# Optimization experiments

Hardware: AMD Instinct MI355X
Metric: run time of the kernel (lower is better)

## Reference

```python
import jax, jax.numpy as jnp
import numpy as np

H = 256            # hidden_size
S = 4              # num_of_steps
B = 512            # reactions
N_MOLS = B * S     # 2048 molecules
ATOMS_PER_MOL = 32
N_ATOMS = N_MOLS * ATOMS_PER_MOL   # 65536
BONDS_PER_MOL = 64
N_BONDS = N_MOLS * BONDS_PER_MOL   # 131072 directed bonds (+1 pad row)
MAX_NB = 6
ATOM_FDIM = 133
BOND_FDIM = 147
DEPTH = 3
N_ITERS = 3  # Set2Set iterations


def setup_inputs() -> dict:
    key = jax.random.key(0)
    ks = jax.random.split(key, 20)
    def p(k, shape):
        return jax.random.normal(k, shape, jnp.float32) * 0.02
    inp = {}
    inp['f_atoms'] = jax.random.normal(ks[0], (N_ATOMS, ATOM_FDIM), jnp.float32)
    f_bonds = jax.random.normal(ks[1], (N_BONDS + 1, BOND_FDIM), jnp.float32)
    inp['f_bonds'] = f_bonds.at[0].set(0.0)  # chemprop zero pad row
    inp['a2b'] = jax.random.randint(ks[2], (N_ATOMS, MAX_NB), 0, N_BONDS + 1)
    inp['b2a'] = jax.random.randint(ks[3], (N_BONDS + 1,), 0, N_ATOMS)
    inp['b2revb'] = jax.random.randint(ks[4], (N_BONDS + 1,), 0, N_BONDS + 1)
    # MPN weights (bias=False for W_i/W_h as in args.bias default)
    inp['W_i'] = p(ks[5], (BOND_FDIM, H))
    inp['W_h'] = p(ks[6], (H, H))
    inp['W_o'] = p(ks[7], (ATOM_FDIM + H, H)); inp['b_o'] = jnp.zeros((H,), jnp.float32)
    # NNAttention over steps
    inp['W_nn0'] = p(ks[8], (2 * H, H));  inp['b_nn0'] = jnp.zeros((H,), jnp.float32)
    inp['W_nn0s'] = p(ks[9], (H, H));     inp['b_nn0s'] = jnp.zeros((H,), jnp.float32)
    inp['W_nn1'] = p(ks[10], (S * H, H)); inp['b_nn1'] = jnp.zeros((H,), jnp.float32)
    # node Set2Set (LSTM: input 2H -> hidden H) + condenser
    inp['lstm_n_Wih'] = p(ks[11], (4 * H, 2 * H))
    inp['lstm_n_Whh'] = p(ks[12], (4 * H, H))
    inp['lstm_n_b'] = jnp.zeros((4 * H,), jnp.float32)
    inp['node_cond_W'] = p(ks[13], (2 * H, H)); inp['node_cond_b'] = jnp.zeros((H,), jnp.float32)
    # graph (step) Set2Set + condenser
    inp['lstm_g_Wih'] = p(ks[14], (4 * H, 2 * H))
    inp['lstm_g_Whh'] = p(ks[15], (4 * H, H))
    inp['lstm_g_b'] = jnp.zeros((4 * H,), jnp.float32)
    inp['graph_cond_W'] = p(ks[16], (2 * H, H)); inp['graph_cond_b'] = jnp.zeros((H,), jnp.float32)
    return inp


def set2set(feat, Wih, Whh, b):
    # feat: [M, N, D]; LSTM n_layers=1, PyTorch gate order i,f,g,o
    M, N, D = feat.shape
    h = jnp.zeros((M, D), feat.dtype)
    c = jnp.zeros((M, D), feat.dtype)
    q_star = jnp.zeros((M, 2 * D), feat.dtype)
    for _ in range(N_ITERS):
        gates = q_star @ Wih.T + h @ Whh.T + b
        i, f, g, o = jnp.split(gates, 4, axis=-1)
        c = jax.nn.sigmoid(f) * c + jax.nn.sigmoid(i) * jnp.tanh(g)
        h = jax.nn.sigmoid(o) * jnp.tanh(c)
        q = h
        alpha = jax.nn.softmax(jnp.einsum('md,mnd->mn', q, feat), axis=1)
        readout = jnp.einsum('mn,mnd->md', alpha, feat)
        q_star = jnp.concatenate([q, readout], axis=-1)
    return q_star


def nn_attention(h, W0, b0, W0s, b0s, W1, b1):
    # vectorized form of the Attention module's s1/s2 double loop
    Bm, Sm, D = h.shape
    h1 = jnp.broadcast_to(h[:, :, None, :], (Bm, Sm, Sm, D))
    h2 = jnp.broadcast_to(h[:, None, :, :], (Bm, Sm, Sm, D))
    pair = jnp.concatenate([h1, h2], -1) @ W0 + b0          # [B,S,S,D] NN0(cat(h_s1,h_s2))
    self_o = h @ W0s + b0s                                   # [B,S,D]   NN0_self(h_s1)
    diag = jnp.eye(Sm, dtype=bool)[None, :, :, None]
    out = jnp.where(diag, self_o[:, :, None, :], pair)       # diagonal uses NN0_self
    return out.reshape(Bm, Sm, Sm * D) @ W1 + b1             # NN1 over s2-concat


def reference(f_atoms, f_bonds, a2b, b2a, b2revb, W_i, W_h, W_o, b_o,
              W_nn0, b_nn0, W_nn0s, b_nn0s, W_nn1, b_nn1,
              lstm_n_Wih, lstm_n_Whh, lstm_n_b, node_cond_W, node_cond_b,
              lstm_g_Wih, lstm_g_Whh, lstm_g_b, graph_cond_W, graph_cond_b):
    # --- bond message passing (chemprop, atom_messages=False) ---
    inp = f_bonds @ W_i                       # [NB+1, H], row 0 = 0 (no bias)
    message = jax.nn.relu(inp)
    message = message.at[0].set(0.0)          # keep pad row zero
    for _ in range(DEPTH - 1):
        a_message = message[a2b].sum(axis=1)          # gather+sum: [NA, H]
        msg = a_message[b2a] - message[b2revb]        # [NB+1, H]
        message = jax.nn.relu(inp + msg @ W_h)
        message = message.at[0].set(0.0)
    nei = message[a2b].sum(axis=1)                    # [NA, H]
    atom_h = jax.nn.relu(jnp.concatenate([f_atoms, nei], -1) @ W_o + b_o)
    # --- node readout: Set2Set per molecule + condenser ---
    feat = atom_h.reshape(N_MOLS, ATOMS_PER_MOL, H)
    mol = set2set(feat, lstm_n_Wih, lstm_n_Whh, lstm_n_b) @ node_cond_W + node_cond_b
    # --- step attention (NNAttention over num_of_steps) ---
    steps = mol.reshape(B, S, H)
    steps = nn_attention(steps, W_nn0, b_nn0, W_nn0s, b_nn0s, W_nn1, b_nn1)
    # --- step readout: Set2Set over steps + condenser ---
    out = set2set(steps, lstm_g_Wih, lstm_g_Whh, lstm_g_b) @ graph_cond_W + graph_cond_b
    return out  # [B, H]
```

## Files before the change

kernel.cpp:

```cpp
#include <hip/hip_runtime.h>
#include <math.h>

#define H 256
#define S_STEPS 4
#define B_RXN 512
#define N_MOLS 2048
#define ATOMS_PER_MOL 32
#define N_ATOMS 65536
#define N_BONDS 131072
#define NBP1 131073
#define MAX_NB 6
#define ATOM_FDIM 133
#define BOND_FDIM 147
#define DEPTH 3
#define N_ITERS 3

typedef unsigned short bf16u;
typedef __attribute__((ext_vector_type(8))) short short8v;
typedef __attribute__((ext_vector_type(4))) float f32x4;

__device__ __forceinline__ float b2f(bf16u u) {
    union { unsigned int i; float f; } c; c.i = ((unsigned int)u) << 16; return c.f;
}
__device__ __forceinline__ bf16u f2b(float f) {
    union { float f; unsigned int i; } c; c.f = f;
    unsigned int i = c.i;
    return (bf16u)((i + 0x7FFFu + ((i >> 16) & 1u)) >> 16);
}
__device__ __forceinline__ unsigned int relu2bf(unsigned int w) {
    unsigned int lo = w & 0xFFFFu, hi = w >> 16;
    if (lo & 0x8000u) lo = 0u;
    if (hi & 0x8000u) hi = 0u;
    return lo | (hi << 16);
}

template<int MODE, bool RELUA>
__global__ __launch_bounds__(512) void dense_gemm_k(
    const bf16u* __restrict__ A1,
    const bf16u* __restrict__ A2,
    const bf16u* __restrict__ WT,
    const float* __restrict__ bias,
    bf16u* __restrict__ outb,
    int M)
{
    constexpr int KP = (MODE == 0) ? 160 : ((MODE == 1) ? 256 : 416);
    __shared__ bf16u As[128][40];
    __shared__ bf16u Bs[256][40];

    const int tid = threadIdx.x;
    const int lane = tid & 63, w = tid >> 6;
    const int wr = w >> 2, wc = w & 3;
    const int m0 = blockIdx.x * 128;
    const int ar = tid >> 2, q8 = (tid & 3) * 8;
    const int br = tid >> 1, bh = (tid & 1) * 16;
    const int arow = m0 + ar;
    const bool rok = arow < M;
    const int lr = lane & 15, lk = (lane >> 4) * 8;
    const uint4 z4 = {0u, 0u, 0u, 0u};

    f32x4 acc[4][4];
    const f32x4 zf = {0.f, 0.f, 0.f, 0.f};
    #pragma unroll
    for (int i = 0; i < 4; ++i)
        #pragma unroll
        for (int j = 0; j < 4; ++j) acc[i][j] = zf;

    for (int k0 = 0; k0 < KP; k0 += 32) {
        const int kc = k0 + q8;
        uint4 va;
        if (MODE == 2) {
            va = (kc < 160) ? *(const uint4*)(A1 + (size_t)arow * 160 + kc)
                            : *(const uint4*)(A2 + (size_t)arow * 256 + (kc - 160));
        } else {
            constexpr int LDA = (MODE == 0) ? 160 : 256;
            va = rok ? *(const uint4*)(A1 + (size_t)arow * LDA + kc) : z4;
        }
        if (RELUA) {
            va.x = relu2bf(va.x); va.y = relu2bf(va.y);
            va.z = relu2bf(va.z); va.w = relu2bf(va.w);
        }
        *(uint4*)&As[ar][q8] = va;
        {
            const bf16u* bp = WT + (size_t)br * KP + k0 + bh;
            uint4 b0 = *(const uint4*)(bp);
            uint4 b1 = *(const uint4*)(bp + 8);
            *(uint4*)&Bs[br][bh] = b0;
            *(uint4*)&Bs[br][bh + 8] = b1;
        }
        __syncthreads();

        short8v a[4], b[4];
        #pragma unroll
        for (int mf = 0; mf < 4; ++mf)
            a[mf] = *(const short8v*)&As[wr * 64 + mf * 16 + lr][lk];
        #pragma unroll
        for (int nf = 0; nf < 4; ++nf)
            b[nf] = *(const short8v*)&Bs[wc * 64 + nf * 16 + lr][lk];
        #pragma unroll
        for (int mf = 0; mf < 4; ++mf)
            #pragma unroll
            for (int nf = 0; nf < 4; ++nf)
                acc[mf][nf] = __builtin_amdgcn_mfma_f32_16x16x32_bf16(
                    a[mf], b[nf], acc[mf][nf], 0, 0, 0);
        __syncthreads();
    }

    const int rbase = (lane >> 4) * 4;
    #pragma unroll
    for (int mf = 0; mf < 4; ++mf) {
        #pragma unroll
        for (int nf = 0; nf < 4; ++nf) {
            const int col = wc * 64 + nf * 16 + lr;
            #pragma unroll
            for (int r = 0; r < 4; ++r) {
                const int row = m0 + wr * 64 + mf * 16 + rbase + r;
                if (row >= M) continue;
                float v = acc[mf][nf][r];
                const size_t off = (size_t)row * H + col;
                if (MODE == 2) {
                    v += bias[col];
                    outb[off] = f2b(fmaxf(v, 0.f));
                } else {
                    outb[off] = f2b(v);
                }
            }
        }
    }
}

__global__ __launch_bounds__(256) void combine_k(
    const bf16u* __restrict__ inp, const bf16u* __restrict__ AP,
    const bf16u* __restrict__ MW,
    const int* __restrict__ b2a, const int* __restrict__ b2revb,
    bf16u* __restrict__ msg)
{
    int idx = blockIdx.x * 256 + threadIdx.x;
    if (idx >= NBP1 * 32) return;
    int b = idx >> 5, c = (idx & 31) * 8;
    bf16u* op = msg + (size_t)b * H + c;
    if (b == 0) {
        *(uint4*)op = make_uint4(0u, 0u, 0u, 0u);
        return;
    }
    int a = b2a[b], rb = b2revb[b];
    uint4 ui = *(const uint4*)(inp + (size_t)b * H + c);
    uint4 up = *(const uint4*)(AP + (size_t)a * H + c);
    uint4 um = *(const uint4*)(MW + (size_t)rb * H + c);
    uint4 o;
    unsigned int* pi = &ui.x; unsigned int* pp = &up.x;
    unsigned int* pm = &um.x; unsigned int* po = &o.x;
    #pragma unroll
    for (int t = 0; t < 4; ++t) {
        float lo = b2f((bf16u)(pi[t] & 0xFFFFu)) + b2f((bf16u)(pp[t] & 0xFFFFu))
                 - b2f((bf16u)(pm[t] & 0xFFFFu));
        float hi = b2f((bf16u)(pi[t] >> 16)) + b2f((bf16u)(pp[t] >> 16))
                 - b2f((bf16u)(pm[t] >> 16));
        lo = fmaxf(lo, 0.f); hi = fmaxf(hi, 0.f);
        po[t] = (unsigned int)f2b(lo) | ((unsigned int)f2b(hi) << 16);
    }
    *(uint4*)op = o;
}

template<bool BIAS>
__global__ __launch_bounds__(256) void lin64_k(
    const float* __restrict__ A1, int lda1, int KA1,
    const float* __restrict__ A2, int lda2,
    const bf16u* __restrict__ WT, int ldw,
    const float* __restrict__ bias,
    float* __restrict__ C, int ldc, int K)
{
    __shared__ bf16u As[64][40];
    __shared__ bf16u Bs[64][40];
    const int tid = threadIdx.x;
    const int lane = tid & 63, w = tid >> 6;
    const int m0 = blockIdx.x * 64;
    const int col0 = blockIdx.y * 64;
    const int ar = tid >> 2, kq8 = (tid & 3) * 8;
    const int lr = lane & 15, lk = (lane >> 4) * 8;

    f32x4 acc[4];
    const f32x4 zf = {0.f, 0.f, 0.f, 0.f};
    #pragma unroll
    for (int j = 0; j < 4; ++j) acc[j] = zf;

    for (int k0 = 0; k0 < K; k0 += 32) {
        const float* src = (k0 < KA1)
            ? (A1 + (size_t)(m0 + ar) * lda1 + k0 + kq8)
            : (A2 + (size_t)(m0 + ar) * lda2 + (k0 - KA1) + kq8);
        float4 f0 = *(const float4*)src;
        float4 f1 = *(const float4*)(src + 4);
        ushort4 s0, s1;
        s0.x = f2b(f0.x); s0.y = f2b(f0.y); s0.z = f2b(f0.z); s0.w = f2b(f0.w);
        s1.x = f2b(f1.x); s1.y = f2b(f1.y); s1.z = f2b(f1.z); s1.w = f2b(f1.w);
        *(ushort4*)&As[ar][kq8] = s0;
        *(ushort4*)&As[ar][kq8 + 4] = s1;
        *(uint4*)&Bs[ar][kq8] = *(const uint4*)(WT + (size_t)(col0 + ar) * ldw + k0 + kq8);
        __syncthreads();

        short8v a = *(const short8v*)&As[w * 16 + lr][lk];
        short8v b[4];
        #pragma unroll
        for (int nf = 0; nf < 4; ++nf)
            b[nf] = *(const short8v*)&Bs[nf * 16 + lr][lk];
        #pragma unroll
        for (int nf = 0; nf < 4; ++nf)
            acc[nf] = __builtin_amdgcn_mfma_f32_16x16x32_bf16(a, b[nf], acc[nf], 0, 0, 0);
        __syncthreads();
    }

    const int rbase = (lane >> 4) * 4;
    #pragma unroll
    for (int nf = 0; nf < 4; ++nf) {
        const int col = col0 + nf * 16 + lr;
        #pragma unroll
        for (int r = 0; r < 4; ++r) {
            const int row = m0 + w * 16 + rbase + r;
            float v = acc[nf][r];
            if (BIAS) v += bias[col];
            C[(size_t)row * ldc + col] = v;
        }
    }
}

__global__ __launch_bounds__(256) void prep_wt_k(const float* __restrict__ W,
                                                 bf16u* __restrict__ WT, int K, int KP)
{
    int idx = blockIdx.x * 256 + threadIdx.x;
    if (idx >= 256 * KP) return;
    int n = idx / KP, k = idx - n * KP;
    WT[idx] = (k < K) ? f2b(W[(size_t)k * H + n]) : (bf16u)0;
}

__global__ __launch_bounds__(256) void prep_wto_k(const float* __restrict__ Wo,
                                                  bf16u* __restrict__ WT)
{
    int idx = blockIdx.x * 256 + threadIdx.x;
    if (idx >= 256 * 416) return;
    int n = idx / 416, k = idx - n * 416;
    float v = 0.f;
    if (k < ATOM_FDIM) v = Wo[(size_t)k * H + n];
    else if (k >= 160) v = Wo[(size_t)(ATOM_FDIM + k - 160) * H + n];
    WT[idx] = f2b(v);
}

__global__ __launch_bounds__(256) void prep_wt_t_k(const float* __restrict__ W,
                                                   bf16u* __restrict__ WT, int K)
{
    int idx = blockIdx.x * 256 + threadIdx.x;
    if (idx >= 256 * K) return;
    int n = idx / K, k = idx - n * K;
    WT[idx] = f2b(W[(size_t)k * 256 + n]);
}

__global__ __launch_bounds__(256) void prep_wt_gates_k(const float* __restrict__ Wih,
                                                       const float* __restrict__ Whh,
                                                       bf16u* __restrict__ WT)
{
    int idx = blockIdx.x * 256 + threadIdx.x;
    if (idx >= 1024 * 768) return;
    int n = idx / 768, k = idx - n * 768;
    WT[idx] = f2b(k < 512 ? Wih[(size_t)n * 512 + k] : Whh[(size_t)n * 256 + (k - 512)]);
}

__global__ __launch_bounds__(256) void prep_wt_pqs_k(const float* __restrict__ Wnn0,
                                                     const float* __restrict__ Wnn0s,
                                                     bf16u* __restrict__ WT,
                                                     float* __restrict__ bias_pqs,
                                                     const float* __restrict__ b_nn0s)
{
    int idx = blockIdx.x * 256 + threadIdx.x;
    if (idx < 768) bias_pqs[idx] = (idx < 512) ? 0.f : b_nn0s[idx - 512];
    if (idx >= 768 * 256) return;
    int n = idx / 256, k = idx - n * 256;
    float v;
    if (n < 256)      v = Wnn0[(size_t)k * 256 + n];
    else if (n < 512) v = Wnn0[(size_t)(256 + k) * 256 + (n - 256)];
    else              v = Wnn0s[(size_t)k * 256 + (n - 512)];
    WT[idx] = f2b(v);
}

__global__ __launch_bounds__(256) void prep_feat16_k(const float* __restrict__ F,
                                                     bf16u* __restrict__ O,
                                                     int rows, int K)
{
    int idx = blockIdx.x * 256 + threadIdx.x;
    if (idx >= rows * 160) return;
    int r = idx / 160, c = idx - r * 160;
    O[idx] = (c < K) ? f2b(F[(size_t)r * K + c]) : (bf16u)0;
}

__global__ __launch_bounds__(256) void gather6_bf16_k(const bf16u* __restrict__ msg,
                                                      const int* __restrict__ a2b,
                                                      bf16u* __restrict__ outb)
{
    int idx = blockIdx.x * 256 + threadIdx.x;
    if (idx >= N_ATOMS * (H / 8)) return;
    int na = idx >> 5, c = idx & 31;
    const int* nb = a2b + (size_t)na * MAX_NB;
    float s[8] = {0.f, 0.f, 0.f, 0.f, 0.f, 0.f, 0.f, 0.f};
    #pragma unroll
    for (int j = 0; j < MAX_NB; ++j) {
        uint4 u = *(const uint4*)(msg + (size_t)nb[j] * H + c * 8);
        s[0] += b2f((bf16u)(u.x & 0xFFFFu)); s[1] += b2f((bf16u)(u.x >> 16));
        s[2] += b2f((bf16u)(u.y & 0xFFFFu)); s[3] += b2f((bf16u)(u.y >> 16));
        s[4] += b2f((bf16u)(u.z & 0xFFFFu)); s[5] += b2f((bf16u)(u.z >> 16));
        s[6] += b2f((bf16u)(u.w & 0xFFFFu)); s[7] += b2f((bf16u)(u.w >> 16));
    }
    uint4 o;
    o.x = (unsigned int)f2b(s[0]) | ((unsigned int)f2b(s[1]) << 16);
    o.y = (unsigned int)f2b(s[2]) | ((unsigned int)f2b(s[3]) << 16);
    o.z = (unsigned int)f2b(s[4]) | ((unsigned int)f2b(s[5]) << 16);
    o.w = (unsigned int)f2b(s[6]) | ((unsigned int)f2b(s[7]) << 16);
    *(uint4*)(outb + (size_t)na * H + c * 8) = o;
}

__global__ __launch_bounds__(256) void zero_f32_k(float* __restrict__ p, int n)
{
    int idx = blockIdx.x * 256 + threadIdx.x;
    if (idx < n) p[idx] = 0.f;
}

__device__ __forceinline__ float sigm(float x) { return 1.f / (1.f + expf(-x)); }

__global__ __launch_bounds__(256) void lstm_pw_k(const float* __restrict__ gates,
                                                 float* __restrict__ h,
                                                 float* __restrict__ c, int M)
{
    int idx = blockIdx.x * 256 + threadIdx.x;
    if (idx >= M * H) return;
    int m = idx >> 8, d = idx & 255;
    const float* g = gates + (size_t)m * (4 * H);
    float ig = sigm(g[d]);
    float fg = sigm(g[H + d]);
    float gg = tanhf(g[2 * H + d]);
    float og = sigm(g[3 * H + d]);
    float cn = fg * c[idx] + ig * gg;
    c[idx] = cn;
    h[idx] = og * tanhf(cn);
}

template<bool BF16F>
__global__ __launch_bounds__(256) void s2s_attn_k(const void* __restrict__ featv,
                                                  const float* __restrict__ h,
                                                  float* __restrict__ q_star, int Nn)
{
    int m = blockIdx.x;
    int t = threadIdx.x;
    int lane = t & 63, wave = t >> 6;
    __shared__ float sc[32];
    const bf16u* fb = (const bf16u*)featv;
    const float* ff = (const float*)featv;
    const size_t fbase = (size_t)m * Nn * H;
    const float* hm = h + (size_t)m * H;
    for (int n = wave; n < Nn; n += 4) {
        float p = 0.f;
        if (BF16F) {
            ushort4 u = *(const ushort4*)(fb + fbase + (size_t)n * H + lane * 4);
            const float4 h4 = *(const float4*)(hm + lane * 4);
            p = b2f(u.x) * h4.x + b2f(u.y) * h4.y + b2f(u.z) * h4.z + b2f(u.w) * h4.w;
        } else {
            const float* fr = ff + fbase + (size_t)n * H;
            #pragma unroll
            for (int u = 0; u < 4; ++u) p += fr[lane * 4 + u] * hm[lane * 4 + u];
        }
        #pragma unroll
        for (int o = 32; o >= 1; o >>= 1) p += __shfl_xor(p, o);
        if (lane == 0) sc[n] = p;
    }
    __syncthreads();
    float mx = -1e30f;
    for (int n = 0; n < Nn; ++n) mx = fmaxf(mx, sc[n]);
    float ssum = 0.f, r = 0.f;
    for (int n = 0; n < Nn; ++n) {
        float a = expf(sc[n] - mx);
        ssum += a;
        float fv = BF16F ? b2f(fb[fbase + (size_t)n * H + t]) : ff[fbase + (size_t)n * H + t];
        r += a * fv;
    }
    r /= ssum;
    q_star[(size_t)m * (2 * H) + t] = hm[t];
    q_star[(size_t)m * (2 * H) + H + t] = r;
}

__global__ __launch_bounds__(256) void build_x_k(const float* __restrict__ PQS,
                                                 const float* __restrict__ b0,
                                                 float* __restrict__ X)
{
    int idx = blockIdx.x * 256 + threadIdx.x;
    if (idx >= B_RXN * S_STEPS * S_STEPS * H) return;
    int d  = idx & 255;
    int s2 = (idx >> 8) & 3;
    int s1 = (idx >> 10) & 3;
    int b  = idx >> 12;
    float v;
    if (s1 == s2) v = PQS[((size_t)(b * S_STEPS + s1)) * 768 + 512 + d];
    else v = PQS[((size_t)(b * S_STEPS + s1)) * 768 + d]
           + PQS[((size_t)(b * S_STEPS + s2)) * 768 + 256 + d] + b0[d];
    X[idx] = v;
}

extern "C" void kernel_launch(void* const* d_in, const int* in_sizes, int n_in,
                              void* d_out, int out_size, void* d_ws, size_t ws_size,
                              hipStream_t stream)
{
    const float* f_atoms   = (const float*)d_in[0];
    const float* f_bonds   = (const float*)d_in[1];
    const int*   a2b       = (const int*)d_in[2];
    const int*   b2a       = (const int*)d_in[3];
    const int*   b2revb    = (const int*)d_in[4];
    const float* W_i       = (const float*)d_in[5];
    const float* W_h       = (const float*)d_in[6];
    const float* W_o       = (const float*)d_in[7];
    const float* b_o       = (const float*)d_in[8];
    const float* W_nn0     = (const float*)d_in[9];
    const float* b_nn0     = (const float*)d_in[10];
    const float* W_nn0s    = (const float*)d_in[11];
    const float* b_nn0s    = (const float*)d_in[12];
    const float* W_nn1     = (const float*)d_in[13];
    const float* b_nn1     = (const float*)d_in[14];
    const float* lstm_n_Wih = (const float*)d_in[15];
    const float* lstm_n_Whh = (const float*)d_in[16];
    const float* lstm_n_b   = (const float*)d_in[17];
    const float* node_cond_W = (const float*)d_in[18];
    const float* node_cond_b = (const float*)d_in[19];
    const float* lstm_g_Wih = (const float*)d_in[20];
    const float* lstm_g_Whh = (const float*)d_in[21];
    const float* lstm_g_b   = (const float*)d_in[22];
    const float* graph_cond_W = (const float*)d_in[23];
    const float* graph_cond_b = (const float*)d_in[24];
    float* out = (float*)d_out;

    const size_t SZB = (size_t)NBP1 * H * sizeof(bf16u);
    char* base = (char*)d_ws;
    bf16u* INP  = (bf16u*)(base);
    bf16u* MSG  = (bf16u*)(base + SZB);
    bf16u* MW   = (bf16u*)(base + 2 * SZB);
    bf16u* AMSG = (bf16u*)(base + 3 * SZB);
    bf16u* WT_I = (bf16u*)(base + 3 * SZB + 33554432);
    bf16u* WT_H = (bf16u*)(base + 3 * SZB + 33636352);
    bf16u* WT_O = (bf16u*)(base + 3 * SZB + 33767424);
    bf16u* FB16 = MW;
    bf16u* FA16 = MW;
    bf16u* ATOMH16 = (bf16u*)(base);
    float* SMALL = (float*)(base + SZB);
    float* GATES  = SMALL;
    float* HN     = SMALL + 2097152;
    float* CN     = SMALL + 2621440;
    float* QSTARN = SMALL + 3145728;
    float* MOL    = SMALL + 4194304;
    float* PQS    = SMALL + 4718592;
    float* XBUF   = SMALL + 6291456;
    float* STEPS  = SMALL + 8388608;
    float* HG     = SMALL + 8912896;
    float* CG     = SMALL + 9043968;
    float* QSTARG = SMALL + 9175040;
    float* GATESG = SMALL + 9437184;
    char* sm2 = base + 2 * SZB + 25165824;
    bf16u* WTG_N   = (bf16u*)(sm2);
    bf16u* WTG_G   = (bf16u*)(sm2 + 1572864);
    bf16u* WT_NC   = (bf16u*)(sm2 + 3145728);
    bf16u* WT_PQS  = (bf16u*)(sm2 + 3407872);
    bf16u* WT_N1   = (bf16u*)(sm2 + 3801088);
    bf16u* WT_GC   = (bf16u*)(sm2 + 4325376);
    float* BIAS_PQS = (float*)(sm2 + 4587520);

    dim3 blk(256), blk5(512);
    const int MB_BOND = (NBP1 + 127) / 128;
    const int MB_ATOM = N_ATOMS / 128;
    const int G_GATH = (N_ATOMS * (H / 8) + 255) / 256;
    const int G_COMB = (NBP1 * 32 + 255) / 256;

    prep_wt_k<<<(256 * 160 + 255) / 256, blk, 0, stream>>>(W_i, WT_I, BOND_FDIM, 160);
    prep_wt_k<<<(256 * 256 + 255) / 256, blk, 0, stream>>>(W_h, WT_H, H, 256);
    prep_wto_k<<<(256 * 416 + 255) / 256, blk, 0, stream>>>(W_o, WT_O);
    prep_feat16_k<<<(int)(((size_t)NBP1 * 160 + 255) / 256), blk, 0, stream>>>(
        f_bonds, FB16, NBP1, BOND_FDIM);

    dense_gemm_k<0, false><<<MB_BOND, blk5, 0, stream>>>(
        FB16, nullptr, WT_I, nullptr, INP, NBP1);

    dense_gemm_k<1, true><<<MB_BOND, blk5, 0, stream>>>(
        INP, nullptr, WT_H, nullptr, MW, NBP1);
    gather6_bf16_k<<<G_GATH, blk, 0, stream>>>(MW, a2b, AMSG);
    combine_k<<<G_COMB, blk, 0, stream>>>(INP, AMSG, MW, b2a, b2revb, MSG);
    dense_gemm_k<1, false><<<MB_BOND, blk5, 0, stream>>>(
        MSG, nullptr, WT_H, nullptr, MW, NBP1);
    gather6_bf16_k<<<G_GATH, blk, 0, stream>>>(MW, a2b, AMSG);
    combine_k<<<G_COMB, blk, 0, stream>>>(INP, AMSG, MW, b2a, b2revb, MSG);

    gather6_bf16_k<<<G_GATH, blk, 0, stream>>>(MSG, a2b, AMSG);

    prep_feat16_k<<<(N_ATOMS * 160 + 255) / 256, blk, 0, stream>>>(
        f_atoms, FA16, N_ATOMS, ATOM_FDIM);
    prep_wt_gates_k<<<(1024 * 768 + 255) / 256, blk, 0, stream>>>(lstm_n_Wih, lstm_n_Whh, WTG_N);
    prep_wt_gates_k<<<(1024 * 768 + 255) / 256, blk, 0, stream>>>(lstm_g_Wih, lstm_g_Whh, WTG_G);
    prep_wt_t_k<<<(256 * 512 + 255) / 256, blk, 0, stream>>>(node_cond_W, WT_NC, 512);
    prep_wt_pqs_k<<<(768 * 256 + 255) / 256, blk, 0, stream>>>(W_nn0, W_nn0s, WT_PQS, BIAS_PQS, b_nn0s);
    prep_wt_t_k<<<(256 * 1024 + 255) / 256, blk, 0, stream>>>(W_nn1, WT_N1, 1024);
    prep_wt_t_k<<<(256 * 512 + 255) / 256, blk, 0, stream>>>(graph_cond_W, WT_GC, 512);

    dense_gemm_k<2, false><<<MB_ATOM, blk5, 0, stream>>>(
        FA16, AMSG, WT_O, b_o, ATOMH16, N_ATOMS);

    zero_f32_k<<<(2097152 + 255) / 256, blk, 0, stream>>>(HN, 2097152);
    for (int it = 0; it < N_ITERS; ++it) {
        lin64_k<true><<<dim3(N_MOLS / 64, 16), blk, 0, stream>>>(
            QSTARN, 2 * H, 2 * H, HN, H, WTG_N, 3 * H, lstm_n_b, GATES, 4 * H, 3 * H);
        lstm_pw_k<<<(N_MOLS * H) / 256, blk, 0, stream>>>(GATES, HN, CN, N_MOLS);
        s2s_attn_k<true><<<N_MOLS, blk, 0, stream>>>(ATOMH16, HN, QSTARN, ATOMS_PER_MOL);
    }
    lin64_k<true><<<dim3(N_MOLS / 64, 4), blk, 0, stream>>>(
        QSTARN, 2 * H, 2 * H, QSTARN, 2 * H, WT_NC, 2 * H, node_cond_b, MOL, H, 2 * H);

    lin64_k<true><<<dim3(N_MOLS / 64, 12), blk, 0, stream>>>(
        MOL, H, H, MOL, H, WT_PQS, H, BIAS_PQS, PQS, 3 * H, H);
    build_x_k<<<(B_RXN * 16 * H) / 256, blk, 0, stream>>>(PQS, b_nn0, XBUF);
    lin64_k<true><<<dim3(N_MOLS / 64, 4), blk, 0, stream>>>(
        XBUF, S_STEPS * H, S_STEPS * H, XBUF, S_STEPS * H, WT_N1, S_STEPS * H, b_nn1,
        STEPS, H, S_STEPS * H);

    zero_f32_k<<<(524288 + 255) / 256, blk, 0, stream>>>(HG, 524288);
    for (int it = 0; it < N_ITERS; ++it) {
        lin64_k<true><<<dim3(B_RXN / 64, 16), blk, 0, stream>>>(
            QSTARG, 2 * H, 2 * H, HG, H, WTG_G, 3 * H, lstm_g_b, GATESG, 4 * H, 3 * H);
        lstm_pw_k<<<(B_RXN * H) / 256, blk, 0, stream>>>(GATESG, HG, CG, B_RXN);
        s2s_attn_k<false><<<B_RXN, blk, 0, stream>>>(STEPS, HG, QSTARG, S_STEPS);
    }

    lin64_k<true><<<dim3(B_RXN / 64, 4), blk, 0, stream>>>(
        QSTARG, 2 * H, 2 * H, QSTARG, 2 * H, WT_GC, 2 * H, graph_cond_b, out, H, 2 * H);
}
```

Baseline: 681.2 us.

## Prefetch dense GEMM tiles, fuse LSTM gates with pointwise, merge weight prep

The dense bond/atom GEMM now loads the next K-slice into registers while the MFMAs run on the current shared-memory tile, so global-load latency overlaps compute at the cost of an extra barrier per step. The Set2Set LSTM gate GEMM and pointwise cell update are fused into one kernel that groups the i/f/g/o columns per block and ping-pongs h/c buffers. This removes the gates buffer round trip and one launch per iteration. The six weight-prep kernels are merged into a single launch to cut launch overhead.

```diff
diff --git a/kernel.cpp b/kernel.cpp
--- a/kernel.cpp
+++ b/kernel.cpp
@@ -44,6 +44,7 @@
     int M)
 {
     constexpr int KP = (MODE == 0) ? 160 : ((MODE == 1) ? 256 : 416);
+    constexpr int NS = KP / 32;
     __shared__ bf16u As[128][40];
     __shared__ bf16u Bs[256][40];
 
@@ -58,36 +59,42 @@
     const int lr = lane & 15, lk = (lane >> 4) * 8;
     const uint4 z4 = {0u, 0u, 0u, 0u};
 
-    f32x4 acc[4][4];
-    const f32x4 zf = {0.f, 0.f, 0.f, 0.f};
-    #pragma unroll
-    for (int i = 0; i < 4; ++i)
-        #pragma unroll
-        for (int j = 0; j < 4; ++j) acc[i][j] = zf;
-
-    for (int k0 = 0; k0 < KP; k0 += 32) {
-        const int kc = k0 + q8;
-        uint4 va;
+    auto loadA = [&](int s) -> uint4 {
+        const int kc = s * 32 + q8;
         if (MODE == 2) {
-            va = (kc < 160) ? *(const uint4*)(A1 + (size_t)arow * 160 + kc)
-                            : *(const uint4*)(A2 + (size_t)arow * 256 + (kc - 160));
+            return (kc < 160) ? *(const uint4*)(A1 + (size_t)arow * 160 + kc)
+                              : *(const uint4*)(A2 + (size_t)arow * 256 + (kc - 160));
         } else {
             constexpr int LDA = (MODE == 0) ? 160 : 256;
-            va = rok ? *(const uint4*)(A1 + (size_t)arow * LDA + kc) : z4;
-        }
+            return rok ? *(const uint4*)(A1 + (size_t)arow * LDA + kc) : z4;
+        }
+    };
+    auto loadB0 = [&](int s) { return *(const uint4*)(WT + (size_t)br * KP + s * 32 + bh); };
+    auto loadB1 = [&](int s) { return *(const uint4*)(WT + (size_t)br * KP + s * 32 + bh + 8); };
+    auto writeAB = [&](uint4 va, uint4 vb0, uint4 vb1) {
         if (RELUA) {
             va.x = relu2bf(va.x); va.y = relu2bf(va.y);
             va.z = relu2bf(va.z); va.w = relu2bf(va.w);
         }
         *(uint4*)&As[ar][q8] = va;
-        {
-            const bf16u* bp = WT + (size_t)br * KP + k0 + bh;
-            uint4 b0 = *(const uint4*)(bp);
-            uint4 b1 = *(const uint4*)(bp + 8);
-            *(uint4*)&Bs[br][bh] = b0;
-            *(uint4*)&Bs[br][bh + 8] = b1;
-        }
-        __syncthreads();
+        *(uint4*)&Bs[br][bh] = vb0;
+        *(uint4*)&Bs[br][bh + 8] = vb1;
+    };
+
+    f32x4 acc[4][4];
+    const f32x4 zf = {0.f, 0.f, 0.f, 0.f};
+    #pragma unroll
+    for (int i = 0; i < 4; ++i)
+        #pragma unroll
+        for (int j = 0; j < 4; ++j) acc[i][j] = zf;
+
+    writeAB(loadA(0), loadB0(0), loadB1(0));
+    __syncthreads();
+
+    for (int s = 0; s < NS; ++s) {
+        const bool pf = (s + 1 < NS);
+        uint4 va = z4, vb0 = z4, vb1 = z4;
+        if (pf) { va = loadA(s + 1); vb0 = loadB0(s + 1); vb1 = loadB1(s + 1); }
 
         short8v a[4], b[4];
         #pragma unroll
@@ -103,6 +110,10 @@
                 acc[mf][nf] = __builtin_amdgcn_mfma_f32_16x16x32_bf16(
                     a[mf], b[nf], acc[mf][nf], 0, 0, 0);
         __syncthreads();
+        if (pf) {
+            writeAB(va, vb0, vb1);
+            __syncthreads();
+        }
     }
 
     const int rbase = (lane >> 4) * 4;
@@ -222,6 +233,75 @@
     }
 }
 
+__device__ __forceinline__ float sigm(float x) { return 1.f / (1.f + expf(-x)); }
+
+__global__ __launch_bounds__(256) void gates_lstm_k(
+    const float* __restrict__ QSTAR,
+    const float* __restrict__ Hc,
+    const float* __restrict__ Cc,
+    const bf16u* __restrict__ WT,
+    const float* __restrict__ bias,
+    float* __restrict__ Hn,
+    float* __restrict__ Cn,
+    int M)
+{
+    __shared__ bf16u As[64][40];
+    __shared__ bf16u Bs[64][40];
+    const int tid = threadIdx.x;
+    const int lane = tid & 63, w = tid >> 6;
+    const int m0 = blockIdx.x * 64;
+    const int db = blockIdx.y;
+    const int ar = tid >> 2, q8 = (tid & 3) * 8;
+    const int lr = lane & 15, lk = (lane >> 4) * 8;
+
+    f32x4 acc[4];
+    const f32x4 zf = {0.f, 0.f, 0.f, 0.f};
+    #pragma unroll
+    for (int g = 0; g < 4; ++g) acc[g] = zf;
+
+    for (int k0 = 0; k0 < 768; k0 += 32) {
+        const float* src = (k0 < 512)
+            ? QSTAR + (size_t)(m0 + ar) * 512 + k0 + q8
+            : Hc + (size_t)(m0 + ar) * 256 + (k0 - 512) + q8;
+        float4 f0 = *(const float4*)src;
+        float4 f1 = *(const float4*)(src + 4);
+        ushort4 s0, s1;
+        s0.x = f2b(f0.x); s0.y = f2b(f0.y); s0.z = f2b(f0.z); s0.w = f2b(f0.w);
+        s1.x = f2b(f1.x); s1.y = f2b(f1.y); s1.z = f2b(f1.z); s1.w = f2b(f1.w);
+        *(ushort4*)&As[ar][q8] = s0;
+        *(ushort4*)&As[ar][q8 + 4] = s1;
+        {
+            int rho = tid >> 2;
+            int g = rho >> 4, cn = rho & 15;
+            *(uint4*)&Bs[rho][q8] =
+                *(const uint4*)(WT + (size_t)(g * 256 + db * 16 + cn) * 768 + k0 + q8);
+        }
+        __syncthreads();
+        short8v a = *(const short8v*)&As[w * 16 + lr][lk];
+        #pragma unroll
+        for (int g = 0; g < 4; ++g) {
+            short8v b = *(const short8v*)&Bs[g * 16 + lr][lk];
+            acc[g] = __builtin_amdgcn_mfma_f32_16x16x32_bf16(a, b, acc[g], 0, 0, 0);
+        }
+        __syncthreads();
+    }
+
+    const int rbase = (lane >> 4) * 4;
+    const int d = db * 16 + lr;
+    const float bi = bias[d], bf = bias[256 + d], bg = bias[512 + d], bo = bias[768 + d];
+    #pragma unroll
+    for (int r = 0; r < 4; ++r) {
+        const int row = m0 + w * 16 + rbase + r;
+        float i_ = acc[0][r] + bi;
+        float f_ = acc[1][r] + bf;
+        float g_ = acc[2][r] + bg;
+        float o_ = acc[3][r] + bo;
+        float cv = sigm(f_) * Cc[(size_t)row * 256 + d] + sigm(i_) * tanhf(g_);
+        Cn[(size_t)row * 256 + d] = cv;
+        Hn[(size_t)row * 256 + d] = sigm(o_) * tanhf(cv);
+    }
+}
+
 __global__ __launch_bounds__(256) void prep_wt_k(const float* __restrict__ W,
                                                  bf16u* __restrict__ WT, int K, int KP)
 {
@@ -243,41 +323,66 @@
     WT[idx] = f2b(v);
 }
 
-__global__ __launch_bounds__(256) void prep_wt_t_k(const float* __restrict__ W,
-                                                   bf16u* __restrict__ WT, int K)
-{
-    int idx = blockIdx.x * 256 + threadIdx.x;
-    if (idx >= 256 * K) return;
-    int n = idx / K, k = idx - n * K;
-    WT[idx] = f2b(W[(size_t)k * 256 + n]);
-}
-
-__global__ __launch_bounds__(256) void prep_wt_gates_k(const float* __restrict__ Wih,
-                                                       const float* __restrict__ Whh,
-                                                       bf16u* __restrict__ WT)
-{
-    int idx = blockIdx.x * 256 + threadIdx.x;
-    if (idx >= 1024 * 768) return;
-    int n = idx / 768, k = idx - n * 768;
-    WT[idx] = f2b(k < 512 ? Wih[(size_t)n * 512 + k] : Whh[(size_t)n * 256 + (k - 512)]);
-}
-
-__global__ __launch_bounds__(256) void prep_wt_pqs_k(const float* __restrict__ Wnn0,
-                                                     const float* __restrict__ Wnn0s,
-                                                     bf16u* __restrict__ WT,
-                                                     float* __restrict__ bias_pqs,
-                                                     const float* __restrict__ b_nn0s)
-{
-    int idx = blockIdx.x * 256 + threadIdx.x;
-    if (idx < 768) bias_pqs[idx] = (idx < 512) ? 0.f : b_nn0s[idx - 512];
-    if (idx >= 768 * 256) return;
-    int n = idx / 256, k = idx - n * 256;
-    float v;
-    if (n < 256)      v = Wnn0[(size_t)k * 256 + n];
-    else if (n < 512) v = Wnn0[(size_t)(256 + k) * 256 + (n - 256)];
-    else              v = Wnn0s[(size_t)k * 256 + (n - 512)];
-    WT[idx] = f2b(v);
-}
+#define SZ_WTG   786432
+#define SZ_WTNC  131072
+#define SZ_WTPQS 196608
+#define SZ_WTN1  262144
+#define SZ_WTGC  131072
+__global__ __launch_bounds__(256) void prep_mid_k(
+    const float* __restrict__ Wih_n, const float* __restrict__ Whh_n,
+    const float* __restrict__ Wih_g, const float* __restrict__ Whh_g,
+    const float* __restrict__ ncW,  const float* __restrict__ Wnn0,
+    const float* __restrict__ Wnn0s, const float* __restrict__ Wnn1,
+    const float* __restrict__ gcW,  const float* __restrict__ b_nn0s,
+    bf16u* __restrict__ WTG_N, bf16u* __restrict__ WTG_G,
+    bf16u* __restrict__ WT_NC, bf16u* __restrict__ WT_PQS,
+    bf16u* __restrict__ WT_N1, bf16u* __restrict__ WT_GC,
+    float* __restrict__ BIAS_PQS)
+{
+    int idx = blockIdx.x * 256 + threadIdx.x;
+    if (idx < SZ_WTG) {
+        int n = idx / 768, k = idx - n * 768;
+        WTG_N[idx] = f2b(k < 512 ? Wih_n[(size_t)n * 512 + k] : Whh_n[(size_t)n * 256 + (k - 512)]);
+        return;
+    }
+    idx -= SZ_WTG;
+    if (idx < SZ_WTG) {
+        int n = idx / 768, k = idx - n * 768;
+        WTG_G[idx] = f2b(k < 512 ? Wih_g[(size_t)n * 512 + k] : Whh_g[(size_t)n * 256 + (k - 512)]);
+        return;
+    }
+    idx -= SZ_WTG;
+    if (idx < SZ_WTNC) {
+        int n = idx / 512, k = idx - n * 512;
+        WT_NC[idx] = f2b(ncW[(size_t)k * 256 + n]);
+        return;
+    }
+    idx -= SZ_WTNC;
+    if (idx < SZ_WTPQS) {
+        int n = idx / 256, k = idx - n * 256;
+        float v;
+        if (n < 256)      v = Wnn0[(size_t)k * 256 + n];
+        else if (n < 512) v = Wnn0[(size_t)(256 + k) * 256 + (n - 256)];
+        else              v = Wnn0s[(size_t)k * 256 + (n - 512)];
+        WT_PQS[idx] = f2b(v);
+        return;
+    }
+    idx -= SZ_WTPQS;
+    if (idx < SZ_WTN1) {
+        int n = idx / 1024, k = idx - n * 1024;
+        WT_N1[idx] = f2b(Wnn1[(size_t)k * 256 + n]);
+        return;
+    }
+    idx -= SZ_WTN1;
+    if (idx < SZ_WTGC) {
+        int n = idx / 512, k = idx - n * 512;
+        WT_GC[idx] = f2b(gcW[(size_t)k * 256 + n]);
+        return;
+    }
+    idx -= SZ_WTGC;
+    if (idx < 768) BIAS_PQS[idx] = (idx < 512) ? 0.f : b_nn0s[idx - 512];
+}
+#define PREP_MID_TOTAL (2 * SZ_WTG + SZ_WTNC + SZ_WTPQS + SZ_WTN1 + SZ_WTGC + 768)
 
 __global__ __launch_bounds__(256) void prep_feat16_k(const float* __restrict__ F,
                                                      bf16u* __restrict__ O,
@@ -318,25 +423,6 @@
 {
     int idx = blockIdx.x * 256 + threadIdx.x;
     if (idx < n) p[idx] = 0.f;
-}
-
-__device__ __forceinline__ float sigm(float x) { return 1.f / (1.f + expf(-x)); }
-
-__global__ __launch_bounds__(256) void lstm_pw_k(const float* __restrict__ gates,
-                                                 float* __restrict__ h,
-                                                 float* __restrict__ c, int M)
-{
-    int idx = blockIdx.x * 256 + threadIdx.x;
-    if (idx >= M * H) return;
-    int m = idx >> 8, d = idx & 255;
-    const float* g = gates + (size_t)m * (4 * H);
-    float ig = sigm(g[d]);
-    float fg = sigm(g[H + d]);
-    float gg = tanhf(g[2 * H + d]);
-    float og = sigm(g[3 * H + d]);
-    float cn = fg * c[idx] + ig * gg;
-    c[idx] = cn;
-    h[idx] = og * tanhf(cn);
 }
 
 template<bool BF16F>
@@ -443,7 +529,6 @@
     bf16u* FA16 = MW;
     bf16u* ATOMH16 = (bf16u*)(base);
     float* SMALL = (float*)(base + SZB);
-    float* GATES  = SMALL;
     float* HN     = SMALL + 2097152;
     float* CN     = SMALL + 2621440;
     float* QSTARN = SMALL + 3145728;
@@ -454,7 +539,10 @@
     float* HG     = SMALL + 8912896;
     float* CG     = SMALL + 9043968;
     float* QSTARG = SMALL + 9175040;
-    float* GATESG = SMALL + 9437184;
+    float* HN2    = SMALL + 10485760;
+    float* CN2    = SMALL + 11010048;
+    float* HG2    = SMALL + 11534336;
+    float* CG2    = SMALL + 11665408;
     char* sm2 = base + 2 * SZB + 25165824;
     bf16u* WTG_N   = (bf16u*)(sm2);
     bf16u* WTG_G   = (bf16u*)(sm2 + 1572864);
@@ -492,22 +580,25 @@
 
     prep_feat16_k<<<(N_ATOMS * 160 + 255) / 256, blk, 0, stream>>>(
         f_atoms, FA16, N_ATOMS, ATOM_FDIM);
-    prep_wt_gates_k<<<(1024 * 768 + 255) / 256, blk, 0, stream>>>(lstm_n_Wih, lstm_n_Whh, WTG_N);
-    prep_wt_gates_k<<<(1024 * 768 + 255) / 256, blk, 0, stream>>>(lstm_g_Wih, lstm_g_Whh, WTG_G);
-    prep_wt_t_k<<<(256 * 512 + 255) / 256, blk, 0, stream>>>(node_cond_W, WT_NC, 512);
-    prep_wt_pqs_k<<<(768 * 256 + 255) / 256, blk, 0, stream>>>(W_nn0, W_nn0s, WT_PQS, BIAS_PQS, b_nn0s);
-    prep_wt_t_k<<<(256 * 1024 + 255) / 256, blk, 0, stream>>>(W_nn1, WT_N1, 1024);
-    prep_wt_t_k<<<(256 * 512 + 255) / 256, blk, 0, stream>>>(graph_cond_W, WT_GC, 512);
+    prep_mid_k<<<(PREP_MID_TOTAL + 255) / 256, blk, 0, stream>>>(
+        lstm_n_Wih, lstm_n_Whh, lstm_g_Wih, lstm_g_Whh,
+        node_cond_W, W_nn0, W_nn0s, W_nn1, graph_cond_W, b_nn0s,
+        WTG_N, WTG_G, WT_NC, WT_PQS, WT_N1, WT_GC, BIAS_PQS);
 
     dense_gemm_k<2, false><<<MB_ATOM, blk5, 0, stream>>>(
         FA16, AMSG, WT_O, b_o, ATOMH16, N_ATOMS);
 
     zero_f32_k<<<(2097152 + 255) / 256, blk, 0, stream>>>(HN, 2097152);
-    for (int it = 0; it < N_ITERS; ++it) {
-        lin64_k<true><<<dim3(N_MOLS / 64, 16), blk, 0, stream>>>(
-            QSTARN, 2 * H, 2 * H, HN, H, WTG_N, 3 * H, lstm_n_b, GATES, 4 * H, 3 * H);
-        lstm_pw_k<<<(N_MOLS * H) / 256, blk, 0, stream>>>(GATES, HN, CN, N_MOLS);
-        s2s_attn_k<true><<<N_MOLS, blk, 0, stream>>>(ATOMH16, HN, QSTARN, ATOMS_PER_MOL);
+    {
+        float *hc = HN, *cc = CN, *hn = HN2, *cn = CN2;
+        for (int it = 0; it < N_ITERS; ++it) {
+            gates_lstm_k<<<dim3(N_MOLS / 64, 16), blk, 0, stream>>>(
+                QSTARN, hc, cc, WTG_N, lstm_n_b, hn, cn, N_MOLS);
+            s2s_attn_k<true><<<N_MOLS, blk, 0, stream>>>(ATOMH16, hn, QSTARN, ATOMS_PER_MOL);
+            float* t;
+            t = hc; hc = hn; hn = t;
+            t = cc; cc = cn; cn = t;
+        }
     }
     lin64_k<true><<<dim3(N_MOLS / 64, 4), blk, 0, stream>>>(
         QSTARN, 2 * H, 2 * H, QSTARN, 2 * H, WT_NC, 2 * H, node_cond_b, MOL, H, 2 * H);
@@ -520,11 +611,16 @@
         STEPS, H, S_STEPS * H);
 
     zero_f32_k<<<(524288 + 255) / 256, blk, 0, stream>>>(HG, 524288);
-    for (int it = 0; it < N_ITERS; ++it) {
-        lin64_k<true><<<dim3(B_RXN / 64, 16), blk, 0, stream>>>(
-            QSTARG, 2 * H, 2 * H, HG, H, WTG_G, 3 * H, lstm_g_b, GATESG, 4 * H, 3 * H);
-        lstm_pw_k<<<(B_RXN * H) / 256, blk, 0, stream>>>(GATESG, HG, CG, B_RXN);
-        s2s_attn_k<false><<<B_RXN, blk, 0, stream>>>(STEPS, HG, QSTARG, S_STEPS);
+    {
+        float *hc = HG, *cc = CG, *hn = HG2, *cn = CG2;
+        for (int it = 0; it < N_ITERS; ++it) {
+            gates_lstm_k<<<dim3(B_RXN / 64, 16), blk, 0, stream>>>(
+                QSTARG, hc, cc, WTG_G, lstm_g_b, hn, cn, B_RXN);
+            s2s_attn_k<false><<<B_RXN, blk, 0, stream>>>(STEPS, hn, QSTARG, S_STEPS);
+            float* t;
+            t = hc; hc = hn; hn = t;
+            t = cc; cc = cn; cn = t;
+        }
     }
 
     lin64_k<true><<<dim3(B_RXN / 64, 4), blk, 0, stream>>>(
```

After: 676.9 us. No clear change (-0.6%).
